# Kernel tuning notes

Hardware: AMD Instinct MI355X
Metric: run time of the kernel (lower is better)

The kernel has to match this reference:

```python
import jax, jax.numpy as jnp
import numpy as np

NUM_NODES = 100000
NUM_EDGES = 1600000
INPUT_DIM = 128
HIDDEN_DIM = 64
OUTPUT_DIM = 2
DROPOUT_P = 0.5


def setup_inputs() -> dict:
    key = jax.random.key(0)
    ks = jax.random.split(key, 6)
    x = jax.random.normal(ks[0], (NUM_NODES, INPUT_DIM), dtype=jnp.float32)
    edge_index = jax.random.randint(ks[1], (2, NUM_EDGES), 0, NUM_NODES, dtype=jnp.int64)
    W_conv = jax.random.normal(ks[2], (INPUT_DIM, HIDDEN_DIM), dtype=jnp.float32) * (1.0 / np.sqrt(INPUT_DIM))
    b_conv = jax.random.normal(ks[3], (HIDDEN_DIM,), dtype=jnp.float32) * 0.02
    W_lin = jax.random.normal(ks[4], (HIDDEN_DIM, OUTPUT_DIM), dtype=jnp.float32) * (1.0 / np.sqrt(HIDDEN_DIM))
    b_lin = jax.random.normal(ks[5], (OUTPUT_DIM,), dtype=jnp.float32) * 0.02
    return {"x": x, "edge_index": edge_index, "W_conv": W_conv, "b_conv": b_conv,
            "W_lin": W_lin, "b_lin": b_lin}


def _gcn_conv(x, edge_index, W, b):
    n = x.shape[0]
    # linear transform first (PyG GCNConv)
    h = x @ W  # [N, hidden]
    # add self-loops
    loop = jnp.arange(n, dtype=edge_index.dtype)
    row = jnp.concatenate([edge_index[0], loop])  # source
    col = jnp.concatenate([edge_index[1], loop])  # target
    # symmetric normalization deg^{-1/2} (degree counted on targets, incl. self-loops)
    deg = jax.ops.segment_sum(jnp.ones_like(col, dtype=h.dtype), col, num_segments=n)
    dinv = jnp.where(deg > 0, jax.lax.rsqrt(deg), 0.0)
    norm = dinv[row] * dinv[col]  # [E+N]
    # gather -> scale -> scatter-add
    msgs = h[row] * norm[:, None]  # [E+N, hidden]
    out = jax.ops.segment_sum(msgs, col, num_segments=n)
    return out + b


def reference(x, edge_index, W_conv, b_conv, W_lin, b_lin):
    h = _gcn_conv(x, edge_index, W_conv, b_conv)
    h = jax.nn.relu(h)
    # dropout p=0.5, training mode, deterministic key for reproducibility
    keep = jax.random.bernoulli(jax.random.key(42), 1.0 - DROPOUT_P, h.shape)
    h = jnp.where(keep, h / (1.0 - DROPOUT_P), 0.0)
    return h @ W_lin + b_lin
```

## Files before the change

kernel.cpp:

```cpp
#include <hip/hip_runtime.h>
#include <hip/hip_bf16.h>

#define N_NODES 100000
#define N_EDGES 1600000
#define IN_DIM 128
#define HID 64
#define NB ((N_NODES + 255) / 256)
#define EPB 4096
#define BUCKET_BLOCKS ((N_EDGES + EPB - 1) / EPB)
#define MAXPB 8192

typedef __attribute__((ext_vector_type(8))) short bf16x8;
typedef __attribute__((ext_vector_type(4))) float f32x4;

__device__ __forceinline__ unsigned rotl32(unsigned x, unsigned r) {
    return (x << r) | (x >> (32u - r));
}

__device__ __forceinline__ void threefry2x32_k42(unsigned x0, unsigned x1,
                                                 unsigned& o0, unsigned& o1) {
    const unsigned ks0 = 0u;
    const unsigned ks1 = 42u;
    const unsigned ks2 = 0u ^ 42u ^ 0x1BD11BDAu;
    x0 += ks0; x1 += ks1;
    x0 += x1; x1 = rotl32(x1, 13); x1 ^= x0;
    x0 += x1; x1 = rotl32(x1, 15); x1 ^= x0;
    x0 += x1; x1 = rotl32(x1, 26); x1 ^= x0;
    x0 += x1; x1 = rotl32(x1, 6);  x1 ^= x0;
    x0 += ks1; x1 += ks2 + 1u;
    x0 += x1; x1 = rotl32(x1, 17); x1 ^= x0;
    x0 += x1; x1 = rotl32(x1, 29); x1 ^= x0;
    x0 += x1; x1 = rotl32(x1, 16); x1 ^= x0;
    x0 += x1; x1 = rotl32(x1, 24); x1 ^= x0;
    x0 += ks2; x1 += ks0 + 2u;
    x0 += x1; x1 = rotl32(x1, 13); x1 ^= x0;
    x0 += x1; x1 = rotl32(x1, 15); x1 ^= x0;
    x0 += x1; x1 = rotl32(x1, 26); x1 ^= x0;
    x0 += x1; x1 = rotl32(x1, 6);  x1 ^= x0;
    x0 += ks0; x1 += ks1 + 3u;
    x0 += x1; x1 = rotl32(x1, 17); x1 ^= x0;
    x0 += x1; x1 = rotl32(x1, 29); x1 ^= x0;
    x0 += x1; x1 = rotl32(x1, 16); x1 ^= x0;
    x0 += x1; x1 = rotl32(x1, 24); x1 ^= x0;
    x0 += ks1; x1 += ks2 + 4u;
    x0 += x1; x1 = rotl32(x1, 13); x1 ^= x0;
    x0 += x1; x1 = rotl32(x1, 15); x1 ^= x0;
    x0 += x1; x1 = rotl32(x1, 26); x1 ^= x0;
    x0 += x1; x1 = rotl32(x1, 6);  x1 ^= x0;
    x0 += ks2; x1 += ks0 + 5u;
    o0 = x0; o1 = x1;
}

__device__ __forceinline__ float bf2f(unsigned short u) {
    return __uint_as_float((unsigned)u << 16);
}
__device__ __forceinline__ float bf2f_lo(unsigned u) {
    return __uint_as_float(u << 16);
}
__device__ __forceinline__ float bf2f_hi(unsigned u) {
    return __uint_as_float(u & 0xffff0000u);
}

__global__ __launch_bounds__(512) void k_bucket(const int* __restrict__ src,
                                                const int* __restrict__ dst,
                                                int* __restrict__ bucketcnt,
                                                unsigned* __restrict__ gbuf) {
    __shared__ int cnt[512];
    __shared__ int off[512];
    __shared__ int cur[NB];
    __shared__ int gbase[NB];
    __shared__ unsigned buf[EPB];
    __shared__ unsigned short bkt[EPB];
    const int t = threadIdx.x;
    const int e0 = blockIdx.x * EPB;
    const int n = min(EPB, N_EDGES - e0);
    cnt[t] = 0;
    __syncthreads();
    unsigned myrec[EPB / 512];
    int myb[EPB / 512];
#pragma unroll
    for (int k = 0; k < EPB / 512; k++) {
        int e = e0 + k * 512 + t;
        if (e < N_EDGES) {
            int r = src[e];
            int c = dst[e];
            int b = c >> 8;
            myrec[k] = ((unsigned)(c & 255) << 17) | (unsigned)r;
            myb[k] = b;
            atomicAdd(&cnt[b], 1);
        } else {
            myb[k] = -1;
        }
    }
    __syncthreads();
    int own = cnt[t];
    for (int o = 1; o < 512; o <<= 1) {
        int v = (t >= o) ? cnt[t - o] : 0;
        __syncthreads();
        cnt[t] += v;
        __syncthreads();
    }
    off[t] = cnt[t] - own;
    if (t < NB) {
        cur[t] = off[t];
        gbase[t] = t * MAXPB + (own ? atomicAdd(&bucketcnt[t], own) : 0);
    }
    __syncthreads();
#pragma unroll
    for (int k = 0; k < EPB / 512; k++) {
        if (myb[k] >= 0) {
            int p = atomicAdd(&cur[myb[k]], 1);
            buf[p] = myrec[k];
            bkt[p] = (unsigned short)myb[k];
        }
    }
    __syncthreads();
    for (int j = t; j < n; j += 512) {
        int b = bkt[j];
        gbuf[gbase[b] + (j - off[b])] = buf[j];
    }
}

__global__ __launch_bounds__(256) void k_csr3(unsigned* __restrict__ gbuf,
                                              const int* __restrict__ bucketcnt,
                                              int2* __restrict__ row_se,
                                              float* __restrict__ dinv) {
    __shared__ unsigned lbuf[MAXPB];
    __shared__ int lcnt[256];
    __shared__ int pre[256];
    __shared__ int cur[256];
    const int b = blockIdx.x, t = threadIdx.x;
    const int n = bucketcnt[b];
    const unsigned* reg = gbuf + (size_t)b * MAXPB;
    lcnt[t] = 0;
    for (int j = t; j < n; j += 256) lbuf[j] = reg[j];
    __syncthreads();
    for (int j = t; j < n; j += 256) atomicAdd(&lcnt[lbuf[j] >> 17], 1);
    __syncthreads();
    const int my = lcnt[t];
    pre[t] = my;
    __syncthreads();
    for (int o = 1; o < 256; o <<= 1) {
        int v = (t >= o) ? pre[t - o] : 0;
        __syncthreads();
        pre[t] += v;
        __syncthreads();
    }
    const int base = b * MAXPB + pre[t] - my;
    cur[t] = base;
    const int c = b * 256 + t;
    if (c < N_NODES) {
        row_se[c] = make_int2(base, base + my);
        dinv[c] = rsqrtf((float)(my + 1));
    }
    __syncthreads();
    for (int j = t; j < n; j += 256) {
        const unsigned rec = lbuf[j];
        const int pos = atomicAdd(&cur[rec >> 17], 1);
        ((int*)gbuf)[pos] = (int)(rec & 0x1FFFF);
    }
}

__global__ __launch_bounds__(256) void k_gemm(const float* __restrict__ x,
                                              const float* __restrict__ W,
                                              const float* __restrict__ dinv,
                                              unsigned short* __restrict__ gm) {
    __shared__ unsigned short WtH[HID][136];
    __shared__ unsigned short WtL[HID][136];
    const int t = threadIdx.x;
    {
        const int n = t & 63;
        const int k0 = (t >> 6) * 32;
        for (int k = k0; k < k0 + 32; k += 2) {
            float w0 = W[(size_t)k * HID + n];
            float w1 = W[(size_t)(k + 1) * HID + n];
            unsigned short h0 = __bfloat16_as_ushort(__float2bfloat16(w0));
            unsigned short h1 = __bfloat16_as_ushort(__float2bfloat16(w1));
            unsigned short l0 = __bfloat16_as_ushort(__float2bfloat16(w0 - bf2f(h0)));
            unsigned short l1 = __bfloat16_as_ushort(__float2bfloat16(w1 - bf2f(h1)));
            *(unsigned*)&WtH[n][k] = (unsigned)h0 | ((unsigned)h1 << 16);
            *(unsigned*)&WtL[n][k] = (unsigned)l0 | ((unsigned)l1 << 16);
        }
    }
    __syncthreads();

    const int wave = t >> 6, lane = t & 63;
    const int row16 = lane & 15;
    const int kgrp = lane >> 4;
    const int browA = blockIdx.x * 64 + wave * 16;

    const int rA = min(browA + row16, N_NODES - 1);
    const float* xr = x + (size_t)rA * IN_DIM + kgrp * 8;
    float xv[32];
#pragma unroll
    for (int ks = 0; ks < 4; ks++) {
        *(f32x4*)&xv[ks * 8]     = *(const f32x4*)(xr + ks * 32);
        *(f32x4*)&xv[ks * 8 + 4] = *(const f32x4*)(xr + ks * 32 + 4);
    }
    bf16x8 ah[4], al[4];
#pragma unroll
    for (int ks = 0; ks < 4; ks++) {
#pragma unroll
        for (int j = 0; j < 8; j++) {
            float v = xv[ks * 8 + j];
            unsigned short h = __bfloat16_as_ushort(__float2bfloat16(v));
            unsigned short l = __bfloat16_as_ushort(__float2bfloat16(v - bf2f(h)));
            ah[ks][j] = (short)h;
            al[ks][j] = (short)l;
        }
    }

    float dv[4];
    int orow[4];
#pragma unroll
    for (int i = 0; i < 4; i++) {
        orow[i] = browA + kgrp * 4 + i;
        dv[i] = dinv[min(orow[i], N_NODES - 1)];
    }

#pragma unroll
    for (int nt = 0; nt < 4; nt++) {
        const int n = nt * 16 + row16;
        bf16x8 bh[4], bl[4];
#pragma unroll
        for (int ks = 0; ks < 4; ks++) {
            bh[ks] = *(const bf16x8*)&WtH[n][ks * 32 + kgrp * 8];
            bl[ks] = *(const bf16x8*)&WtL[n][ks * 32 + kgrp * 8];
        }
        f32x4 acc = {0.f, 0.f, 0.f, 0.f};
#pragma unroll
        for (int ks = 0; ks < 4; ks++)
            acc = __builtin_amdgcn_mfma_f32_16x16x32_bf16(ah[ks], bh[ks], acc, 0, 0, 0);
#pragma unroll
        for (int ks = 0; ks < 4; ks++)
            acc = __builtin_amdgcn_mfma_f32_16x16x32_bf16(al[ks], bh[ks], acc, 0, 0, 0);
#pragma unroll
        for (int ks = 0; ks < 4; ks++)
            acc = __builtin_amdgcn_mfma_f32_16x16x32_bf16(ah[ks], bl[ks], acc, 0, 0, 0);
#pragma unroll
        for (int i = 0; i < 4; i++) {
            if (orow[i] < N_NODES) {
                float g = acc[i] * dv[i];
                gm[(size_t)orow[i] * HID + nt * 16 + row16] =
                    __bfloat16_as_ushort(__float2bfloat16(g));
            }
        }
    }
}

__global__ __launch_bounds__(256, 4) void k_aggr(const unsigned short* __restrict__ gm,
                                                 const int2* __restrict__ row_se,
                                                 const int* __restrict__ srcs,
                                                 const float* __restrict__ dinv,
                                                 const float* __restrict__ bconv,
                                                 const float* __restrict__ Wlin,
                                                 const float* __restrict__ blin,
                                                 float* __restrict__ out) {
    const int c  = blockIdx.x * 16 + (threadIdx.x >> 4);
    const int d4 = threadIdx.x & 15;
    const int2 se = row_se[c];
    const int beg = se.x;
    const int end = se.y;

    const uint2 s0 = *(const uint2*)(gm + ((size_t)c << 6) + (d4 << 2));
    float a0 = bf2f_lo(s0.x), a1 = bf2f_hi(s0.x);
    float a2 = bf2f_lo(s0.y), a3 = bf2f_hi(s0.y);

#define LOADG(ri) (*(const uint2*)(gm + ((size_t)(ri) << 6) + (d4 << 2)))

    if (beg < end) {
        const int last = end - 1;
        int r[8];
        uint2 wa[8], wb[8];
#pragma unroll
        for (int u = 0; u < 8; u++) r[u] = srcs[min(beg + u, last)];
#pragma unroll
        for (int u = 0; u < 8; u++) wa[u] = LOADG(r[u]);
        bool haveB = (beg + 8 < end);
        if (haveB) {
#pragma unroll
            for (int u = 0; u < 8; u++) r[u] = srcs[min(beg + 8 + u, last)];
#pragma unroll
            for (int u = 0; u < 8; u++) wb[u] = LOADG(r[u]);
        }
        int j = beg;
        while (true) {
#pragma unroll
            for (int u = 0; u < 8; u++) {
                const unsigned m = (j + u < end) ? 0xffffffffu : 0u;
                a0 += bf2f_lo(wa[u].x & m); a1 += bf2f_hi(wa[u].x & m);
                a2 += bf2f_lo(wa[u].y & m); a3 += bf2f_hi(wa[u].y & m);
            }
            j += 8;
            if (!haveB) break;
            const bool haveN = (j + 8 < end);
            if (haveN) {
#pragma unroll
                for (int u = 0; u < 8; u++) r[u] = srcs[min(j + 8 + u, last)];
#pragma unroll
                for (int u = 0; u < 8; u++) wa[u] = LOADG(r[u]);
            }
#pragma unroll
            for (int u = 0; u < 8; u++) {
                const unsigned m = (j + u < end) ? 0xffffffffu : 0u;
                a0 += bf2f_lo(wb[u].x & m); a1 += bf2f_hi(wb[u].x & m);
                a2 += bf2f_lo(wb[u].y & m); a3 += bf2f_hi(wb[u].y & m);
            }
            j += 8;
            if (!haveN) break;
            haveB = (j + 8 < end);
            if (haveB) {
#pragma unroll
                for (int u = 0; u < 8; u++) r[u] = srcs[min(j + 8 + u, last)];
#pragma unroll
                for (int u = 0; u < 8; u++) wb[u] = LOADG(r[u]);
            }
        }
    }
#undef LOADG

    const float dv = dinv[c];
    const float4 bc4 = *(const float4*)(bconv + (d4 << 2));
    float v0 = fmaxf(a0 * dv + bc4.x, 0.f);
    float v1 = fmaxf(a1 * dv + bc4.y, 0.f);
    float v2 = fmaxf(a2 * dv + bc4.z, 0.f);
    float v3 = fmaxf(a3 * dv + bc4.w, 0.f);

    const unsigned ib = (unsigned)(c * HID + (d4 << 2));
    unsigned o0, o1;
    threefry2x32_k42(0u, ib + 0u, o0, o1);
    v0 = ((o0 ^ o1) & 0x80000000u) ? 0.f : v0 * 2.f;
    threefry2x32_k42(0u, ib + 1u, o0, o1);
    v1 = ((o0 ^ o1) & 0x80000000u) ? 0.f : v1 * 2.f;
    threefry2x32_k42(0u, ib + 2u, o0, o1);
    v2 = ((o0 ^ o1) & 0x80000000u) ? 0.f : v2 * 2.f;
    threefry2x32_k42(0u, ib + 3u, o0, o1);
    v3 = ((o0 ^ o1) & 0x80000000u) ? 0.f : v3 * 2.f;

    const float4 wl0 = *(const float4*)(Wlin + (d4 << 3));
    const float4 wl1 = *(const float4*)(Wlin + (d4 << 3) + 4);
    float p0 = v0 * wl0.x + v1 * wl0.z + v2 * wl1.x + v3 * wl1.z;
    float p1 = v0 * wl0.y + v1 * wl0.w + v2 * wl1.y + v3 * wl1.w;

#pragma unroll
    for (int off = 8; off; off >>= 1) {
        p0 += __shfl_xor(p0, off);
        p1 += __shfl_xor(p1, off);
    }
    if (d4 == 0) {
        *(float2*)(out + (size_t)c * 2) = make_float2(p0 + blin[0], p1 + blin[1]);
    }
}

extern "C" void kernel_launch(void* const* d_in, const int* in_sizes, int n_in,
                              void* d_out, int out_size, void* d_ws, size_t ws_size,
                              hipStream_t stream) {
    const float* x  = (const float*)d_in[0];
    const void*  ei = d_in[1];
    const float* Wc = (const float*)d_in[2];
    const float* bc = (const float*)d_in[3];
    const float* Wl = (const float*)d_in[4];
    const float* bl = (const float*)d_in[5];
    for (int i = 0; i < n_in; i++) {
        switch (in_sizes[i]) {
            case N_NODES * IN_DIM:   x  = (const float*)d_in[i]; break;
            case 2 * N_EDGES:
            case 4 * N_EDGES:        ei = d_in[i]; break;
            case IN_DIM * HID:       Wc = (const float*)d_in[i]; break;
            case HID:                bc = (const float*)d_in[i]; break;
            case HID * 2:            Wl = (const float*)d_in[i]; break;
            case 2:                  bl = (const float*)d_in[i]; break;
            default: break;
        }
    }
    float* out = (float*)d_out;

    const int* src = (const int*)ei;
    const int* dst = (const int*)ei + N_EDGES;

    char* ws = (char*)d_ws;
    size_t off = 0;
    unsigned short* gm = (unsigned short*)(ws + off); off += (size_t)N_NODES * HID * 2;
    float* dinv        = (float*)(ws + off);   off += (size_t)N_NODES * 4;
    int2*  row_se      = (int2*)(ws + off);    off += (size_t)N_NODES * 8;
    int*   bucketcnt   = (int*)(ws + off);     off += (size_t)(NB + 64) * 4;
    off = (off + 255) & ~(size_t)255;
    unsigned* gbuf     = (unsigned*)(ws + off); off += (size_t)NB * MAXPB * 4;

    hipMemsetAsync(bucketcnt, 0, (size_t)NB * 4, stream);
    k_bucket<<<BUCKET_BLOCKS, 512, 0, stream>>>(src, dst, bucketcnt, gbuf);
    k_csr3<<<NB, 256, 0, stream>>>(gbuf, bucketcnt, row_se, dinv);
    k_gemm<<<(N_NODES + 63) / 64, 256, 0, stream>>>(x, Wc, dinv, gm);
    k_aggr<<<(N_NODES + 15) / 16, 256, 0, stream>>>(gm, row_se, (const int*)gbuf,
                                                    dinv, bc, Wl, bl, out);
}
```

Before: 174.5 us.

## Fuse bucket, CSR, GEMM and aggregation into one cooperative persistent kernel

Replaces the four-kernel pipeline with a single cooperative kernel that uses grid-wide syncs between the bucketing, CSR+GEMM and aggregation phases. It also fuses the CSR build with the GEMM per 256-node bucket, so dinv comes from LDS, and it moves to 512-thread blocks. Non-cooperative fused kernels are kept as a fallback. The aim is to cut launch gaps and the dinv reload. The cost is occupancy limits from the LDS union, grid sync overhead, and aggregation running over fewer persistent blocks.

```diff
diff --git a/kernel.cpp b/kernel.cpp
--- a/kernel.cpp
+++ b/kernel.cpp
@@ -1,14 +1,17 @@
 #include <hip/hip_runtime.h>
 #include <hip/hip_bf16.h>
+#include <hip/hip_cooperative_groups.h>
+
+namespace cg = cooperative_groups;
 
 #define N_NODES 100000
 #define N_EDGES 1600000
 #define IN_DIM 128
 #define HID 64
-#define NB ((N_NODES + 255) / 256)
+#define NB 391
 #define EPB 4096
-#define BUCKET_BLOCKS ((N_EDGES + EPB - 1) / EPB)
 #define MAXPB 8192
+#define AGGR_VB 3125
 
 typedef __attribute__((ext_vector_type(8))) short bf16x8;
 typedef __attribute__((ext_vector_type(4))) float f32x4;
@@ -60,21 +63,31 @@
 __device__ __forceinline__ float bf2f_hi(unsigned u) {
     return __uint_as_float(u & 0xffff0000u);
 }
-
-__global__ __launch_bounds__(512) void k_bucket(const int* __restrict__ src,
-                                                const int* __restrict__ dst,
-                                                int* __restrict__ bucketcnt,
-                                                unsigned* __restrict__ gbuf) {
-    __shared__ int cnt[512];
-    __shared__ int off[512];
-    __shared__ int cur[NB];
-    __shared__ int gbase[NB];
-    __shared__ unsigned buf[EPB];
-    __shared__ unsigned short bkt[EPB];
+__device__ __forceinline__ uint2 loadg(const unsigned short* __restrict__ gm, int ri, int d4) {
+    return *(const uint2*)(gm + ((size_t)ri << 6) + (d4 << 2));
+}
+
+struct LdsP1 {
+    int cnt[512]; int off[512]; int cur[NB]; int gbase[NB];
+    unsigned buf[EPB]; unsigned short bkt[EPB];
+};
+struct LdsP2 {
+    unsigned lbuf[MAXPB]; int lcnt[256]; int pre[256]; int cur[256];
+};
+struct LdsP3 {
+    unsigned short WtH[HID][136]; unsigned short WtL[HID][136];
+};
+union LdsAll { LdsP1 p1; LdsP2 p2; LdsP3 p3; };
+union LdsCG  { LdsP2 p2; LdsP3 p3; };
+
+__device__ __forceinline__ void phase_bucket(int chunk, const int* __restrict__ src,
+                                             const int* __restrict__ dst,
+                                             int* __restrict__ bucketcnt,
+                                             unsigned* __restrict__ gbuf, LdsP1& L) {
     const int t = threadIdx.x;
-    const int e0 = blockIdx.x * EPB;
+    const int e0 = chunk * EPB;
     const int n = min(EPB, N_EDGES - e0);
-    cnt[t] = 0;
+    L.cnt[t] = 0;
     __syncthreads();
     unsigned myrec[EPB / 512];
     int myb[EPB / 512];
@@ -87,186 +100,187 @@
             int b = c >> 8;
             myrec[k] = ((unsigned)(c & 255) << 17) | (unsigned)r;
             myb[k] = b;
-            atomicAdd(&cnt[b], 1);
+            atomicAdd(&L.cnt[b], 1);
         } else {
             myb[k] = -1;
         }
     }
     __syncthreads();
-    int own = cnt[t];
+    int own = L.cnt[t];
     for (int o = 1; o < 512; o <<= 1) {
-        int v = (t >= o) ? cnt[t - o] : 0;
+        int v = (t >= o) ? L.cnt[t - o] : 0;
         __syncthreads();
-        cnt[t] += v;
+        L.cnt[t] += v;
         __syncthreads();
     }
-    off[t] = cnt[t] - own;
+    L.off[t] = L.cnt[t] - own;
     if (t < NB) {
-        cur[t] = off[t];
-        gbase[t] = t * MAXPB + (own ? atomicAdd(&bucketcnt[t], own) : 0);
+        L.cur[t] = L.off[t];
+        L.gbase[t] = t * MAXPB + (own ? atomicAdd(&bucketcnt[t], own) : 0);
     }
     __syncthreads();
 #pragma unroll
     for (int k = 0; k < EPB / 512; k++) {
         if (myb[k] >= 0) {
-            int p = atomicAdd(&cur[myb[k]], 1);
-            buf[p] = myrec[k];
-            bkt[p] = (unsigned short)myb[k];
+            int p = atomicAdd(&L.cur[myb[k]], 1);
+            L.buf[p] = myrec[k];
+            L.bkt[p] = (unsigned short)myb[k];
         }
     }
     __syncthreads();
     for (int j = t; j < n; j += 512) {
-        int b = bkt[j];
-        gbuf[gbase[b] + (j - off[b])] = buf[j];
-    }
-}
-
-__global__ __launch_bounds__(256) void k_csr3(unsigned* __restrict__ gbuf,
-                                              const int* __restrict__ bucketcnt,
-                                              int2* __restrict__ row_se,
-                                              float* __restrict__ dinv) {
-    __shared__ unsigned lbuf[MAXPB];
-    __shared__ int lcnt[256];
-    __shared__ int pre[256];
-    __shared__ int cur[256];
-    const int b = blockIdx.x, t = threadIdx.x;
+        int b = L.bkt[j];
+        gbuf[L.gbase[b] + (j - L.off[b])] = L.buf[j];
+    }
+    __syncthreads();
+}
+
+__device__ __forceinline__ void phase_csr(int b, unsigned* __restrict__ gbuf,
+                                          const int* __restrict__ bucketcnt,
+                                          int2* __restrict__ row_se,
+                                          float* __restrict__ dinv,
+                                          float* __restrict__ dinvL, LdsP2& L) {
+    const int t = threadIdx.x;
     const int n = bucketcnt[b];
     const unsigned* reg = gbuf + (size_t)b * MAXPB;
-    lcnt[t] = 0;
-    for (int j = t; j < n; j += 256) lbuf[j] = reg[j];
-    __syncthreads();
-    for (int j = t; j < n; j += 256) atomicAdd(&lcnt[lbuf[j] >> 17], 1);
-    __syncthreads();
-    const int my = lcnt[t];
-    pre[t] = my;
+    __syncthreads();
+    if (t < 256) L.lcnt[t] = 0;
+    for (int j = t; j < n; j += 512) L.lbuf[j] = reg[j];
+    __syncthreads();
+    for (int j = t; j < n; j += 512) atomicAdd(&L.lcnt[L.lbuf[j] >> 17], 1);
+    __syncthreads();
+    int my = 0;
+    if (t < 256) { my = L.lcnt[t]; L.pre[t] = my; }
     __syncthreads();
     for (int o = 1; o < 256; o <<= 1) {
-        int v = (t >= o) ? pre[t - o] : 0;
+        int v = 0;
+        if (t < 256 && t >= o) v = L.pre[t - o];
         __syncthreads();
-        pre[t] += v;
+        if (t < 256) L.pre[t] += v;
         __syncthreads();
     }
-    const int base = b * MAXPB + pre[t] - my;
-    cur[t] = base;
-    const int c = b * 256 + t;
-    if (c < N_NODES) {
-        row_se[c] = make_int2(base, base + my);
-        dinv[c] = rsqrtf((float)(my + 1));
-    }
-    __syncthreads();
-    for (int j = t; j < n; j += 256) {
-        const unsigned rec = lbuf[j];
-        const int pos = atomicAdd(&cur[rec >> 17], 1);
+    if (t < 256) {
+        const int base = b * MAXPB + L.pre[t] - my;
+        L.cur[t] = base;
+        const float dv = rsqrtf((float)(my + 1));
+        dinvL[t] = dv;
+        const int c = b * 256 + t;
+        if (c < N_NODES) {
+            row_se[c] = make_int2(base, base + my);
+            dinv[c] = dv;
+        }
+    }
+    __syncthreads();
+    for (int j = t; j < n; j += 512) {
+        const unsigned rec = L.lbuf[j];
+        const int pos = atomicAdd(&L.cur[rec >> 17], 1);
         ((int*)gbuf)[pos] = (int)(rec & 0x1FFFF);
     }
 }
 
-__global__ __launch_bounds__(256) void k_gemm(const float* __restrict__ x,
-                                              const float* __restrict__ W,
-                                              const float* __restrict__ dinv,
-                                              unsigned short* __restrict__ gm) {
-    __shared__ unsigned short WtH[HID][136];
-    __shared__ unsigned short WtL[HID][136];
+__device__ __forceinline__ void phase_gemm(int b, const float* __restrict__ x,
+                                           const float* __restrict__ W,
+                                           unsigned short* __restrict__ gm,
+                                           const float* __restrict__ dinvL, LdsP3& L) {
     const int t = threadIdx.x;
+    __syncthreads();
     {
-        const int n = t & 63;
-        const int k0 = (t >> 6) * 32;
-        for (int k = k0; k < k0 + 32; k += 2) {
-            float w0 = W[(size_t)k * HID + n];
-            float w1 = W[(size_t)(k + 1) * HID + n];
+        const int nn = t & 63;
+        const int k0 = (t >> 6) * 16;
+        for (int k = k0; k < k0 + 16; k += 2) {
+            float w0 = W[(size_t)k * HID + nn];
+            float w1 = W[(size_t)(k + 1) * HID + nn];
             unsigned short h0 = __bfloat16_as_ushort(__float2bfloat16(w0));
             unsigned short h1 = __bfloat16_as_ushort(__float2bfloat16(w1));
             unsigned short l0 = __bfloat16_as_ushort(__float2bfloat16(w0 - bf2f(h0)));
             unsigned short l1 = __bfloat16_as_ushort(__float2bfloat16(w1 - bf2f(h1)));
-            *(unsigned*)&WtH[n][k] = (unsigned)h0 | ((unsigned)h1 << 16);
-            *(unsigned*)&WtL[n][k] = (unsigned)l0 | ((unsigned)l1 << 16);
-        }
-    }
-    __syncthreads();
-
+            *(unsigned*)&L.WtH[nn][k] = (unsigned)h0 | ((unsigned)h1 << 16);
+            *(unsigned*)&L.WtL[nn][k] = (unsigned)l0 | ((unsigned)l1 << 16);
+        }
+    }
+    __syncthreads();
     const int wave = t >> 6, lane = t & 63;
     const int row16 = lane & 15;
     const int kgrp = lane >> 4;
-    const int browA = blockIdx.x * 64 + wave * 16;
-
-    const int rA = min(browA + row16, N_NODES - 1);
-    const float* xr = x + (size_t)rA * IN_DIM + kgrp * 8;
-    float xv[32];
-#pragma unroll
-    for (int ks = 0; ks < 4; ks++) {
-        *(f32x4*)&xv[ks * 8]     = *(const f32x4*)(xr + ks * 32);
-        *(f32x4*)&xv[ks * 8 + 4] = *(const f32x4*)(xr + ks * 32 + 4);
-    }
-    bf16x8 ah[4], al[4];
-#pragma unroll
-    for (int ks = 0; ks < 4; ks++) {
-#pragma unroll
-        for (int j = 0; j < 8; j++) {
-            float v = xv[ks * 8 + j];
-            unsigned short h = __bfloat16_as_ushort(__float2bfloat16(v));
-            unsigned short l = __bfloat16_as_ushort(__float2bfloat16(v - bf2f(h)));
-            ah[ks][j] = (short)h;
-            al[ks][j] = (short)l;
-        }
-    }
-
-    float dv[4];
-    int orow[4];
-#pragma unroll
-    for (int i = 0; i < 4; i++) {
-        orow[i] = browA + kgrp * 4 + i;
-        dv[i] = dinv[min(orow[i], N_NODES - 1)];
-    }
-
-#pragma unroll
-    for (int nt = 0; nt < 4; nt++) {
-        const int n = nt * 16 + row16;
-        bf16x8 bh[4], bl[4];
+#pragma unroll
+    for (int p = 0; p < 2; p++) {
+        const int browA = b * 256 + p * 128 + wave * 16;
+        const int rA = min(browA + row16, N_NODES - 1);
+        const float* xr = x + (size_t)rA * IN_DIM + kgrp * 8;
+        float xv[32];
 #pragma unroll
         for (int ks = 0; ks < 4; ks++) {
-            bh[ks] = *(const bf16x8*)&WtH[n][ks * 32 + kgrp * 8];
-            bl[ks] = *(const bf16x8*)&WtL[n][ks * 32 + kgrp * 8];
-        }
-        f32x4 acc = {0.f, 0.f, 0.f, 0.f};
-#pragma unroll
-        for (int ks = 0; ks < 4; ks++)
-            acc = __builtin_amdgcn_mfma_f32_16x16x32_bf16(ah[ks], bh[ks], acc, 0, 0, 0);
-#pragma unroll
-        for (int ks = 0; ks < 4; ks++)
-            acc = __builtin_amdgcn_mfma_f32_16x16x32_bf16(al[ks], bh[ks], acc, 0, 0, 0);
-#pragma unroll
-        for (int ks = 0; ks < 4; ks++)
-            acc = __builtin_amdgcn_mfma_f32_16x16x32_bf16(ah[ks], bl[ks], acc, 0, 0, 0);
+            *(f32x4*)&xv[ks * 8]     = *(const f32x4*)(xr + ks * 32);
+            *(f32x4*)&xv[ks * 8 + 4] = *(const f32x4*)(xr + ks * 32 + 4);
+        }
+        bf16x8 ah[4], al[4];
+#pragma unroll
+        for (int ks = 0; ks < 4; ks++) {
+#pragma unroll
+            for (int j = 0; j < 8; j++) {
+                float v = xv[ks * 8 + j];
+                unsigned short h = __bfloat16_as_ushort(__float2bfloat16(v));
+                unsigned short l = __bfloat16_as_ushort(__float2bfloat16(v - bf2f(h)));
+                ah[ks][j] = (short)h;
+                al[ks][j] = (short)l;
+            }
+        }
+        float dv[4];
+        int orow[4];
 #pragma unroll
         for (int i = 0; i < 4; i++) {
-            if (orow[i] < N_NODES) {
-                float g = acc[i] * dv[i];
-                gm[(size_t)orow[i] * HID + nt * 16 + row16] =
-                    __bfloat16_as_ushort(__float2bfloat16(g));
-            }
-        }
-    }
-}
-
-__global__ __launch_bounds__(256, 4) void k_aggr(const unsigned short* __restrict__ gm,
-                                                 const int2* __restrict__ row_se,
-                                                 const int* __restrict__ srcs,
-                                                 const float* __restrict__ dinv,
-                                                 const float* __restrict__ bconv,
-                                                 const float* __restrict__ Wlin,
-                                                 const float* __restrict__ blin,
-                                                 float* __restrict__ out) {
-    const int c  = blockIdx.x * 16 + (threadIdx.x >> 4);
-    const int d4 = threadIdx.x & 15;
+            orow[i] = browA + kgrp * 4 + i;
+            dv[i] = dinvL[p * 128 + wave * 16 + kgrp * 4 + i];
+        }
+#pragma unroll
+        for (int nt = 0; nt < 4; nt++) {
+            const int nn = nt * 16 + row16;
+            bf16x8 bh[4], bl[4];
+#pragma unroll
+            for (int ks = 0; ks < 4; ks++) {
+                bh[ks] = *(const bf16x8*)&L.WtH[nn][ks * 32 + kgrp * 8];
+                bl[ks] = *(const bf16x8*)&L.WtL[nn][ks * 32 + kgrp * 8];
+            }
+            f32x4 acc = {0.f, 0.f, 0.f, 0.f};
+#pragma unroll
+            for (int ks = 0; ks < 4; ks++)
+                acc = __builtin_amdgcn_mfma_f32_16x16x32_bf16(ah[ks], bh[ks], acc, 0, 0, 0);
+#pragma unroll
+            for (int ks = 0; ks < 4; ks++)
+                acc = __builtin_amdgcn_mfma_f32_16x16x32_bf16(al[ks], bh[ks], acc, 0, 0, 0);
+#pragma unroll
+            for (int ks = 0; ks < 4; ks++)
+                acc = __builtin_amdgcn_mfma_f32_16x16x32_bf16(ah[ks], bl[ks], acc, 0, 0, 0);
+#pragma unroll
+            for (int i = 0; i < 4; i++) {
+                if (orow[i] < N_NODES) {
+                    float g = acc[i] * dv[i];
+                    gm[(size_t)orow[i] * HID + nt * 16 + row16] =
+                        __bfloat16_as_ushort(__float2bfloat16(g));
+                }
+            }
+        }
+    }
+}
+
+__device__ __forceinline__ void phase_aggr(int vb, const unsigned short* __restrict__ gm,
+                                           const int2* __restrict__ row_se,
+                                           const int* __restrict__ srcs,
+                                           const float* __restrict__ dinv,
+                                           const float* __restrict__ bconv,
+                                           const float* __restrict__ Wlin,
+                                           const float* __restrict__ blin,
+                                           float* __restrict__ out) {
+    const int t = threadIdx.x;
+    const int c  = vb * 32 + (t >> 4);
+    const int d4 = t & 15;
     const int2 se = row_se[c];
     const int beg = se.x;
     const int end = se.y;
 
-    const uint2 s0 = *(const uint2*)(gm + ((size_t)c << 6) + (d4 << 2));
+    const uint2 s0 = loadg(gm, c, d4);
     float a0 = bf2f_lo(s0.x), a1 = bf2f_hi(s0.x);
     float a2 = bf2f_lo(s0.y), a3 = bf2f_hi(s0.y);
-
-#define LOADG(ri) (*(const uint2*)(gm + ((size_t)(ri) << 6) + (d4 << 2)))
 
     if (beg < end) {
         const int last = end - 1;
@@ -275,13 +289,13 @@
 #pragma unroll
         for (int u = 0; u < 8; u++) r[u] = srcs[min(beg + u, last)];
 #pragma unroll
-        for (int u = 0; u < 8; u++) wa[u] = LOADG(r[u]);
+        for (int u = 0; u < 8; u++) wa[u] = loadg(gm, r[u], d4);
         bool haveB = (beg + 8 < end);
         if (haveB) {
 #pragma unroll
             for (int u = 0; u < 8; u++) r[u] = srcs[min(beg + 8 + u, last)];
 #pragma unroll
-            for (int u = 0; u < 8; u++) wb[u] = LOADG(r[u]);
+            for (int u = 0; u < 8; u++) wb[u] = loadg(gm, r[u], d4);
         }
         int j = beg;
         while (true) {
@@ -298,7 +312,7 @@
 #pragma unroll
                 for (int u = 0; u < 8; u++) r[u] = srcs[min(j + 8 + u, last)];
 #pragma unroll
-                for (int u = 0; u < 8; u++) wa[u] = LOADG(r[u]);
+                for (int u = 0; u < 8; u++) wa[u] = loadg(gm, r[u], d4);
             }
 #pragma unroll
             for (int u = 0; u < 8; u++) {
@@ -313,11 +327,10 @@
 #pragma unroll
                 for (int u = 0; u < 8; u++) r[u] = srcs[min(j + 8 + u, last)];
 #pragma unroll
-                for (int u = 0; u < 8; u++) wb[u] = LOADG(r[u]);
-            }
-        }
-    }
-#undef LOADG
+                for (int u = 0; u < 8; u++) wb[u] = loadg(gm, r[u], d4);
+            }
+        }
+    }
 
     const float dv = dinv[c];
     const float4 bc4 = *(const float4*)(bconv + (d4 << 2));
@@ -350,6 +363,68 @@
     if (d4 == 0) {
         *(float2*)(out + (size_t)c * 2) = make_float2(p0 + blin[0], p1 + blin[1]);
     }
+}
+
+__global__ void __launch_bounds__(512) k_all(const int* __restrict__ src,
+                                             const int* __restrict__ dst,
+                                             int* __restrict__ bucketcnt,
+                                             unsigned* __restrict__ gbuf,
+                                             const float* __restrict__ x,
+                                             const float* __restrict__ W,
+                                             unsigned short* __restrict__ gm,
+                                             int2* __restrict__ row_se,
+                                             float* __restrict__ dinv,
+                                             const float* __restrict__ bconv,
+                                             const float* __restrict__ Wlin,
+                                             const float* __restrict__ blin,
+                                             float* __restrict__ out) {
+    __shared__ LdsAll sh;
+    __shared__ float dinvL[256];
+    const int G = gridDim.x;
+    for (int chunk = blockIdx.x; chunk < NB; chunk += G)
+        phase_bucket(chunk, src, dst, bucketcnt, gbuf, sh.p1);
+    __threadfence();
+    cg::this_grid().sync();
+    for (int b = blockIdx.x; b < NB; b += G) {
+        phase_csr(b, gbuf, bucketcnt, row_se, dinv, dinvL, sh.p2);
+        phase_gemm(b, x, W, gm, dinvL, sh.p3);
+    }
+    __threadfence();
+    cg::this_grid().sync();
+    for (int vb = blockIdx.x; vb < AGGR_VB; vb += G)
+        phase_aggr(vb, gm, row_se, (const int*)gbuf, dinv, bconv, Wlin, blin, out);
+}
+
+__global__ void __launch_bounds__(512) k_bucketF(const int* __restrict__ src,
+                                                 const int* __restrict__ dst,
+                                                 int* __restrict__ bucketcnt,
+                                                 unsigned* __restrict__ gbuf) {
+    __shared__ LdsP1 sh;
+    phase_bucket(blockIdx.x, src, dst, bucketcnt, gbuf, sh);
+}
+
+__global__ void __launch_bounds__(512) k_csrgemmF(unsigned* __restrict__ gbuf,
+                                                  const int* __restrict__ bucketcnt,
+                                                  int2* __restrict__ row_se,
+                                                  float* __restrict__ dinv,
+                                                  const float* __restrict__ x,
+                                                  const float* __restrict__ W,
+                                                  unsigned short* __restrict__ gm) {
+    __shared__ LdsCG sh;
+    __shared__ float dinvL[256];
+    phase_csr(blockIdx.x, gbuf, bucketcnt, row_se, dinv, dinvL, sh.p2);
+    phase_gemm(blockIdx.x, x, W, gm, dinvL, sh.p3);
+}
+
+__global__ void __launch_bounds__(512) k_aggrF(const unsigned short* __restrict__ gm,
+                                               const int2* __restrict__ row_se,
+                                               const int* __restrict__ srcs,
+                                               const float* __restrict__ dinv,
+                                               const float* __restrict__ bconv,
+                                               const float* __restrict__ Wlin,
+                                               const float* __restrict__ blin,
+                                               float* __restrict__ out) {
+    phase_aggr(blockIdx.x, gm, row_se, srcs, dinv, bconv, Wlin, blin, out);
 }
 
 extern "C" void kernel_launch(void* const* d_in, const int* in_sizes, int n_in,
@@ -388,9 +463,35 @@
     unsigned* gbuf     = (unsigned*)(ws + off); off += (size_t)NB * MAXPB * 4;
 
     hipMemsetAsync(bucketcnt, 0, (size_t)NB * 4, stream);
-    k_bucket<<<BUCKET_BLOCKS, 512, 0, stream>>>(src, dst, bucketcnt, gbuf);
-    k_csr3<<<NB, 256, 0, stream>>>(gbuf, bucketcnt, row_se, dinv);
-    k_gemm<<<(N_NODES + 63) / 64, 256, 0, stream>>>(x, Wc, dinv, gm);
-    k_aggr<<<(N_NODES + 15) / 16, 256, 0, stream>>>(gm, row_se, (const int*)gbuf,
-                                                    dinv, bc, Wl, bl, out);
-}
+
+    static int coop_grid = -2;
+    if (coop_grid == -2) {
+        int occ = 0;
+        if (hipOccupancyMaxActiveBlocksPerMultiprocessor(&occ, k_all, 512, 0) == hipSuccess
+            && occ > 0) {
+            int g = occ * 256;
+            coop_grid = g < NB ? g : NB;
+        } else {
+            coop_grid = -1;
+        }
+    }
+    bool done = false;
+    if (coop_grid > 0) {
+        void* args[] = {(void*)&src, (void*)&dst, (void*)&bucketcnt, (void*)&gbuf,
+                        (void*)&x, (void*)&Wc, (void*)&gm, (void*)&row_se,
+                        (void*)&dinv, (void*)&bc, (void*)&Wl, (void*)&bl, (void*)&out};
+        if (hipLaunchCooperativeKernel(k_all, dim3(coop_grid), dim3(512),
+                                       args, 0, stream) == hipSuccess) {
+            done = true;
+        } else {
+            (void)hipGetLastError();
+            coop_grid = -1;
+        }
+    }
+    if (!done) {
+        k_bucketF<<<NB, 512, 0, stream>>>(src, dst, bucketcnt, gbuf);
+        k_csrgemmF<<<NB, 512, 0, stream>>>(gbuf, bucketcnt, row_se, dinv, x, Wc, gm);
+        k_aggrF<<<AGGR_VB, 512, 0, stream>>>(gm, row_se, (const int*)gbuf,
+                                             dinv, bc, Wl, bl, out);
+    }
+}
```

New measurement: 180.8 us. +3.6%, slower.

## Fuse CSR build with feature GEMM and precompute split-bf16 weights once

Applied to the files above, without the earlier changes.

Merges the CSR-finalization kernel and the dense x@W kernel into one kernel per 256-node bucket. A shared-memory union reuses the CSR scratch space for the transposed weight tiles, and dinv is read from shared memory instead of global. The hi/lo bf16 split of W is now done once by block 0 of the bucket kernel and copied into each GEMM block, rather than recomputed in every block. This removes one launch and redundant weight conversion, but it cuts GEMM parallelism to 391 blocks of 256 threads, each serially processing four 64-row tiles after the CSR phase.

```diff
diff --git a/kernel.cpp b/kernel.cpp
--- a/kernel.cpp
+++ b/kernel.cpp
@@ -5,10 +5,11 @@
 #define N_EDGES 1600000
 #define IN_DIM 128
 #define HID 64
-#define NB ((N_NODES + 255) / 256)
+#define NB 391
 #define EPB 4096
 #define BUCKET_BLOCKS ((N_EDGES + EPB - 1) / EPB)
 #define MAXPB 8192
+#define WTE (HID * 136)
 
 typedef __attribute__((ext_vector_type(8))) short bf16x8;
 typedef __attribute__((ext_vector_type(4))) float f32x4;
@@ -60,11 +61,17 @@
 __device__ __forceinline__ float bf2f_hi(unsigned u) {
     return __uint_as_float(u & 0xffff0000u);
 }
+__device__ __forceinline__ uint2 loadg(const unsigned short* __restrict__ gm, int ri, int d4) {
+    return *(const uint2*)(gm + ((size_t)ri << 6) + (d4 << 2));
+}
 
 __global__ __launch_bounds__(512) void k_bucket(const int* __restrict__ src,
                                                 const int* __restrict__ dst,
                                                 int* __restrict__ bucketcnt,
-                                                unsigned* __restrict__ gbuf) {
+                                                unsigned* __restrict__ gbuf,
+                                                const float* __restrict__ W,
+                                                unsigned short* __restrict__ WhT,
+                                                unsigned short* __restrict__ WlT) {
     __shared__ int cnt[512];
     __shared__ int off[512];
     __shared__ int cur[NB];
@@ -119,130 +126,135 @@
         int b = bkt[j];
         gbuf[gbase[b] + (j - off[b])] = buf[j];
     }
-}
-
-__global__ __launch_bounds__(256) void k_csr3(unsigned* __restrict__ gbuf,
-                                              const int* __restrict__ bucketcnt,
-                                              int2* __restrict__ row_se,
-                                              float* __restrict__ dinv) {
-    __shared__ unsigned lbuf[MAXPB];
-    __shared__ int lcnt[256];
-    __shared__ int pre[256];
-    __shared__ int cur[256];
+    if (blockIdx.x == 0) {
+        for (int idx = t; idx < IN_DIM * HID; idx += 512) {
+            const int k = idx >> 6, nn = idx & 63;
+            const float w = W[idx];
+            const unsigned short h = __bfloat16_as_ushort(__float2bfloat16(w));
+            const unsigned short l = __bfloat16_as_ushort(__float2bfloat16(w - bf2f(h)));
+            WhT[nn * 136 + k] = h;
+            WlT[nn * 136 + k] = l;
+        }
+    }
+}
+
+__global__ __launch_bounds__(256) void k_csrgemm(unsigned* __restrict__ gbuf,
+                                                 const int* __restrict__ bucketcnt,
+                                                 int2* __restrict__ row_se,
+                                                 float* __restrict__ dinv,
+                                                 const float* __restrict__ x,
+                                                 const unsigned short* __restrict__ WhT,
+                                                 const unsigned short* __restrict__ WlT,
+                                                 unsigned short* __restrict__ gm) {
+    __shared__ union {
+        struct { unsigned lbuf[MAXPB]; int lcnt[256]; int pre[256]; int cur[256]; } c;
+        struct { unsigned short WtH[HID][136]; unsigned short WtL[HID][136]; } g;
+    } sh;
+    __shared__ float dinvL[256];
     const int b = blockIdx.x, t = threadIdx.x;
     const int n = bucketcnt[b];
     const unsigned* reg = gbuf + (size_t)b * MAXPB;
-    lcnt[t] = 0;
-    for (int j = t; j < n; j += 256) lbuf[j] = reg[j];
-    __syncthreads();
-    for (int j = t; j < n; j += 256) atomicAdd(&lcnt[lbuf[j] >> 17], 1);
-    __syncthreads();
-    const int my = lcnt[t];
-    pre[t] = my;
+
+    sh.c.lcnt[t] = 0;
+    for (int j = t; j < n; j += 256) sh.c.lbuf[j] = reg[j];
+    __syncthreads();
+    for (int j = t; j < n; j += 256) atomicAdd(&sh.c.lcnt[sh.c.lbuf[j] >> 17], 1);
+    __syncthreads();
+    const int my = sh.c.lcnt[t];
+    sh.c.pre[t] = my;
     __syncthreads();
     for (int o = 1; o < 256; o <<= 1) {
-        int v = (t >= o) ? pre[t - o] : 0;
+        int v = (t >= o) ? sh.c.pre[t - o] : 0;
         __syncthreads();
-        pre[t] += v;
+        sh.c.pre[t] += v;
         __syncthreads();
     }
-    const int base = b * MAXPB + pre[t] - my;
-    cur[t] = base;
+    const int base = b * MAXPB + sh.c.pre[t] - my;
+    sh.c.cur[t] = base;
+    const float dvv = rsqrtf((float)(my + 1));
+    dinvL[t] = dvv;
     const int c = b * 256 + t;
     if (c < N_NODES) {
         row_se[c] = make_int2(base, base + my);
-        dinv[c] = rsqrtf((float)(my + 1));
+        dinv[c] = dvv;
     }
     __syncthreads();
     for (int j = t; j < n; j += 256) {
-        const unsigned rec = lbuf[j];
-        const int pos = atomicAdd(&cur[rec >> 17], 1);
-        ((int*)gbuf)[pos] = (int)(rec & 0x1FFFF);
-    }
-}
-
-__global__ __launch_bounds__(256) void k_gemm(const float* __restrict__ x,
-                                              const float* __restrict__ W,
-                                              const float* __restrict__ dinv,
-                                              unsigned short* __restrict__ gm) {
-    __shared__ unsigned short WtH[HID][136];
-    __shared__ unsigned short WtL[HID][136];
-    const int t = threadIdx.x;
+        const unsigned rec = sh.c.lbuf[j];
+        const int pos = atomicAdd(&sh.c.cur[rec >> 17], 1);
+        ((int*)gbuf)[pos] = (int)(rec & 0x1FFFFu);
+    }
+    __syncthreads();
+
     {
-        const int n = t & 63;
-        const int k0 = (t >> 6) * 32;
-        for (int k = k0; k < k0 + 32; k += 2) {
-            float w0 = W[(size_t)k * HID + n];
-            float w1 = W[(size_t)(k + 1) * HID + n];
-            unsigned short h0 = __bfloat16_as_ushort(__float2bfloat16(w0));
-            unsigned short h1 = __bfloat16_as_ushort(__float2bfloat16(w1));
-            unsigned short l0 = __bfloat16_as_ushort(__float2bfloat16(w0 - bf2f(h0)));
-            unsigned short l1 = __bfloat16_as_ushort(__float2bfloat16(w1 - bf2f(h1)));
-            *(unsigned*)&WtH[n][k] = (unsigned)h0 | ((unsigned)h1 << 16);
-            *(unsigned*)&WtL[n][k] = (unsigned)l0 | ((unsigned)l1 << 16);
-        }
+        const uint4* s1 = (const uint4*)WhT;
+        uint4* d1 = (uint4*)&sh.g.WtH[0][0];
+        for (int i = t; i < WTE / 8; i += 256) d1[i] = s1[i];
+        const uint4* s2 = (const uint4*)WlT;
+        uint4* d2 = (uint4*)&sh.g.WtL[0][0];
+        for (int i = t; i < WTE / 8; i += 256) d2[i] = s2[i];
     }
     __syncthreads();
 
     const int wave = t >> 6, lane = t & 63;
     const int row16 = lane & 15;
     const int kgrp = lane >> 4;
-    const int browA = blockIdx.x * 64 + wave * 16;
-
-    const int rA = min(browA + row16, N_NODES - 1);
-    const float* xr = x + (size_t)rA * IN_DIM + kgrp * 8;
-    float xv[32];
-#pragma unroll
-    for (int ks = 0; ks < 4; ks++) {
-        *(f32x4*)&xv[ks * 8]     = *(const f32x4*)(xr + ks * 32);
-        *(f32x4*)&xv[ks * 8 + 4] = *(const f32x4*)(xr + ks * 32 + 4);
-    }
-    bf16x8 ah[4], al[4];
-#pragma unroll
-    for (int ks = 0; ks < 4; ks++) {
-#pragma unroll
-        for (int j = 0; j < 8; j++) {
-            float v = xv[ks * 8 + j];
-            unsigned short h = __bfloat16_as_ushort(__float2bfloat16(v));
-            unsigned short l = __bfloat16_as_ushort(__float2bfloat16(v - bf2f(h)));
-            ah[ks][j] = (short)h;
-            al[ks][j] = (short)l;
-        }
-    }
-
-    float dv[4];
-    int orow[4];
-#pragma unroll
-    for (int i = 0; i < 4; i++) {
-        orow[i] = browA + kgrp * 4 + i;
-        dv[i] = dinv[min(orow[i], N_NODES - 1)];
-    }
-
-#pragma unroll
-    for (int nt = 0; nt < 4; nt++) {
-        const int n = nt * 16 + row16;
-        bf16x8 bh[4], bl[4];
+#pragma unroll
+    for (int p = 0; p < 4; p++) {
+        const int browA = b * 256 + p * 64 + wave * 16;
+        const int rA = min(browA + row16, N_NODES - 1);
+        const float* xr = x + (size_t)rA * IN_DIM + kgrp * 8;
+        float xv[32];
 #pragma unroll
         for (int ks = 0; ks < 4; ks++) {
-            bh[ks] = *(const bf16x8*)&WtH[n][ks * 32 + kgrp * 8];
-            bl[ks] = *(const bf16x8*)&WtL[n][ks * 32 + kgrp * 8];
-        }
-        f32x4 acc = {0.f, 0.f, 0.f, 0.f};
-#pragma unroll
-        for (int ks = 0; ks < 4; ks++)
-            acc = __builtin_amdgcn_mfma_f32_16x16x32_bf16(ah[ks], bh[ks], acc, 0, 0, 0);
-#pragma unroll
-        for (int ks = 0; ks < 4; ks++)
-            acc = __builtin_amdgcn_mfma_f32_16x16x32_bf16(al[ks], bh[ks], acc, 0, 0, 0);
-#pragma unroll
-        for (int ks = 0; ks < 4; ks++)
-            acc = __builtin_amdgcn_mfma_f32_16x16x32_bf16(ah[ks], bl[ks], acc, 0, 0, 0);
+            *(f32x4*)&xv[ks * 8]     = *(const f32x4*)(xr + ks * 32);
+            *(f32x4*)&xv[ks * 8 + 4] = *(const f32x4*)(xr + ks * 32 + 4);
+        }
+        bf16x8 ah[4], al[4];
+#pragma unroll
+        for (int ks = 0; ks < 4; ks++) {
+#pragma unroll
+            for (int j = 0; j < 8; j++) {
+                float v = xv[ks * 8 + j];
+                unsigned short h = __bfloat16_as_ushort(__float2bfloat16(v));
+                unsigned short l = __bfloat16_as_ushort(__float2bfloat16(v - bf2f(h)));
+                ah[ks][j] = (short)h;
+                al[ks][j] = (short)l;
+            }
+        }
+        float dv[4];
+        int orow[4];
 #pragma unroll
         for (int i = 0; i < 4; i++) {
-            if (orow[i] < N_NODES) {
-                float g = acc[i] * dv[i];
-                gm[(size_t)orow[i] * HID + nt * 16 + row16] =
-                    __bfloat16_as_ushort(__float2bfloat16(g));
+            orow[i] = browA + kgrp * 4 + i;
+            dv[i] = dinvL[p * 64 + wave * 16 + kgrp * 4 + i];
+        }
+#pragma unroll
+        for (int nt = 0; nt < 4; nt++) {
+            const int nn = nt * 16 + row16;
+            bf16x8 bh[4], bl[4];
+#pragma unroll
+            for (int ks = 0; ks < 4; ks++) {
+                bh[ks] = *(const bf16x8*)&sh.g.WtH[nn][ks * 32 + kgrp * 8];
+                bl[ks] = *(const bf16x8*)&sh.g.WtL[nn][ks * 32 + kgrp * 8];
+            }
+            f32x4 acc = {0.f, 0.f, 0.f, 0.f};
+#pragma unroll
+            for (int ks = 0; ks < 4; ks++)
+                acc = __builtin_amdgcn_mfma_f32_16x16x32_bf16(ah[ks], bh[ks], acc, 0, 0, 0);
+#pragma unroll
+            for (int ks = 0; ks < 4; ks++)
+                acc = __builtin_amdgcn_mfma_f32_16x16x32_bf16(al[ks], bh[ks], acc, 0, 0, 0);
+#pragma unroll
+            for (int ks = 0; ks < 4; ks++)
+                acc = __builtin_amdgcn_mfma_f32_16x16x32_bf16(ah[ks], bl[ks], acc, 0, 0, 0);
+#pragma unroll
+            for (int i = 0; i < 4; i++) {
+                if (orow[i] < N_NODES) {
+                    float g = acc[i] * dv[i];
+                    gm[(size_t)orow[i] * HID + nt * 16 + row16] =
+                        __bfloat16_as_ushort(__float2bfloat16(g));
+                }
             }
         }
     }
@@ -262,11 +274,9 @@
     const int beg = se.x;
     const int end = se.y;
 
-    const uint2 s0 = *(const uint2*)(gm + ((size_t)c << 6) + (d4 << 2));
+    const uint2 s0 = loadg(gm, c, d4);
     float a0 = bf2f_lo(s0.x), a1 = bf2f_hi(s0.x);
     float a2 = bf2f_lo(s0.y), a3 = bf2f_hi(s0.y);
-
-#define LOADG(ri) (*(const uint2*)(gm + ((size_t)(ri) << 6) + (d4 << 2)))
 
     if (beg < end) {
         const int last = end - 1;
@@ -275,13 +285,13 @@
 #pragma unroll
         for (int u = 0; u < 8; u++) r[u] = srcs[min(beg + u, last)];
 #pragma unroll
-        for (int u = 0; u < 8; u++) wa[u] = LOADG(r[u]);
+        for (int u = 0; u < 8; u++) wa[u] = loadg(gm, r[u], d4);
         bool haveB = (beg + 8 < end);
         if (haveB) {
 #pragma unroll
             for (int u = 0; u < 8; u++) r[u] = srcs[min(beg + 8 + u, last)];
 #pragma unroll
-            for (int u = 0; u < 8; u++) wb[u] = LOADG(r[u]);
+            for (int u = 0; u < 8; u++) wb[u] = loadg(gm, r[u], d4);
         }
         int j = beg;
         while (true) {
@@ -298,7 +308,7 @@
 #pragma unroll
                 for (int u = 0; u < 8; u++) r[u] = srcs[min(j + 8 + u, last)];
 #pragma unroll
-                for (int u = 0; u < 8; u++) wa[u] = LOADG(r[u]);
+                for (int u = 0; u < 8; u++) wa[u] = loadg(gm, r[u], d4);
             }
 #pragma unroll
             for (int u = 0; u < 8; u++) {
@@ -313,11 +323,10 @@
 #pragma unroll
                 for (int u = 0; u < 8; u++) r[u] = srcs[min(j + 8 + u, last)];
 #pragma unroll
-                for (int u = 0; u < 8; u++) wb[u] = LOADG(r[u]);
-            }
-        }
-    }
-#undef LOADG
+                for (int u = 0; u < 8; u++) wb[u] = loadg(gm, r[u], d4);
+            }
+        }
+    }
 
     const float dv = dinv[c];
     const float4 bc4 = *(const float4*)(bconv + (d4 << 2));
@@ -385,12 +394,15 @@
     int2*  row_se      = (int2*)(ws + off);    off += (size_t)N_NODES * 8;
     int*   bucketcnt   = (int*)(ws + off);     off += (size_t)(NB + 64) * 4;
     off = (off + 255) & ~(size_t)255;
+    unsigned short* WhT = (unsigned short*)(ws + off); off += (size_t)WTE * 2;
+    off = (off + 255) & ~(size_t)255;
+    unsigned short* WlT = (unsigned short*)(ws + off); off += (size_t)WTE * 2;
+    off = (off + 255) & ~(size_t)255;
     unsigned* gbuf     = (unsigned*)(ws + off); off += (size_t)NB * MAXPB * 4;
 
     hipMemsetAsync(bucketcnt, 0, (size_t)NB * 4, stream);
-    k_bucket<<<BUCKET_BLOCKS, 512, 0, stream>>>(src, dst, bucketcnt, gbuf);
-    k_csr3<<<NB, 256, 0, stream>>>(gbuf, bucketcnt, row_se, dinv);
-    k_gemm<<<(N_NODES + 63) / 64, 256, 0, stream>>>(x, Wc, dinv, gm);
+    k_bucket<<<BUCKET_BLOCKS, 512, 0, stream>>>(src, dst, bucketcnt, gbuf, Wc, WhT, WlT);
+    k_csrgemm<<<NB, 256, 0, stream>>>(gbuf, bucketcnt, row_se, dinv, x, WhT, WlT, gm);
     k_aggr<<<(N_NODES + 15) / 16, 256, 0, stream>>>(gm, row_se, (const int*)gbuf,
                                                     dinv, bc, Wl, bl, out);
 }
```

New measurement: 185.1 us. +6.1%, slower.
